# Performance work log

Hardware: AMD Instinct MI355X
Metric: run time of the kernel (lower is better)

## Reference

```python
import jax, jax.numpy as jnp
import numpy as np

N = 50000          # nodes
E = 800000         # edges (before self-loops)
F_IN, F_HID, F_OUT = 128, 64, 64
NEG_SLOPE_ATT = 0.2   # GATConv internal leaky_relu
NEG_SLOPE_ACT = 0.01  # F.leaky_relu default between layers


def setup_inputs() -> dict:
    key = jax.random.key(0)
    ks = jax.random.split(key, 16)

    def glorot(k, shape):
        fan = float(sum(shape)) if len(shape) > 1 else float(shape[0])
        return jax.random.normal(k, shape, jnp.float32) * (2.0 / fan) ** 0.5

    return {
        "x": jax.random.normal(ks[0], (N, F_IN), jnp.float32),
        "edge_index": jax.random.randint(ks[1], (2, E), 0, N, dtype=jnp.int64),
        "W1": glorot(ks[2], (F_IN, F_HID)),
        "a_src1": glorot(ks[3], (F_HID,)),
        "a_dst1": glorot(ks[4], (F_HID,)),
        "b1": jnp.zeros((F_HID,), jnp.float32),
        "W2": glorot(ks[5], (F_HID, F_HID)),
        "a_src2": glorot(ks[6], (F_HID,)),
        "a_dst2": glorot(ks[7], (F_HID,)),
        "b2": jnp.zeros((F_HID,), jnp.float32),
        "W3": glorot(ks[8], (F_HID, F_OUT)),
        "a_src3": glorot(ks[9], (F_OUT,)),
        "a_dst3": glorot(ks[10], (F_OUT,)),
        "b3": jnp.zeros((F_OUT,), jnp.float32),
    }


def gat_conv(h, src, dst, W, a_src, a_dst, b):
    # Single-head PyG GATConv: project, per-edge scores, segment softmax over dst, scatter-add.
    z = h @ W                              # [N, C]
    e_src = z @ a_src                      # [N]
    e_dst = z @ a_dst                      # [N]
    e = jax.nn.leaky_relu(e_src[src] + e_dst[dst], NEG_SLOPE_ATT)  # [E']
    m = jax.ops.segment_max(e, dst, num_segments=N)
    ex = jnp.exp(e - m[dst])
    denom = jax.ops.segment_sum(ex, dst, num_segments=N)
    alpha = ex / (denom[dst] + 1e-16)      # segment softmax (PyG adds 1e-16)
    out = jax.ops.segment_sum(alpha[:, None] * z[src], dst, num_segments=N) + b
    return out, alpha


def reference(x, edge_index, W1, a_src1, a_dst1, b1, W2, a_src2, a_dst2, b2, W3, a_src3, a_dst3, b3):
    # add_self_loops=True (GATConv default): append (i, i) for every node
    loops = jnp.arange(N, dtype=edge_index.dtype)
    ei = jnp.concatenate([edge_index, jnp.stack([loops, loops])], axis=1)  # [2, E+N]
    src, dst = ei[0], ei[1]

    h = x
    alpha = None
    for (W, asr, ads, b) in ((W1, a_src1, a_dst1, b1),
                             (W2, a_src2, a_dst2, b2),
                             (W3, a_src3, a_dst3, b3)):
        h, alpha = gat_conv(h, src, dst, W, asr, ads, b)
        h = jax.nn.leaky_relu(h, NEG_SLOPE_ACT)
    return (h, ei, alpha)
```

## Files before the change

### kernel.cpp

```cpp
#include <hip/hip_runtime.h>
#include <hip/hip_bf16.h>
#include <hip/hip_fp8.h>

#define NN 50000
#define EE 800000
#define E2 850000
#define F_IN 128
#define F_HID 64
#define NCHUNK ((NN + 255) / 256)
#define NTILE  ((NN + 63) / 64)
#define AGGB 2048

#define PNB 32
#define BCAP 32768
#define PCAP 128
#define PCHUNK 2048
#define PBLOCKS ((EE + PCHUNK - 1) / PCHUNK)
#define SLICEB 64

__device__ __forceinline__ unsigned char f32_to_fp8(float x) {
    __hip_fp8_e4m3 t(x);
    return t.__x;
}
__device__ __forceinline__ float fp8_to_f32(unsigned char b) {
    __hip_fp8_e4m3 t; t.__x = b;
    return (float)t;
}

#if defined(__has_builtin)
#  if __has_builtin(__builtin_amdgcn_cvt_f32_fp8)
#    define CVT_FP8(v, s) __builtin_amdgcn_cvt_f32_fp8((v), (s))
#  endif
#endif
#ifndef CVT_FP8
#  define CVT_FP8(v, s) fp8_to_f32(((v) >> (8 * (s))) & 255)
#endif

__global__ __launch_bounds__(256) void hist_part_kernel(const int* __restrict__ ei,
                                                        int* __restrict__ deg,
                                                        int* __restrict__ bin_cur,
                                                        unsigned long long* __restrict__ bins,
                                                        float* __restrict__ ei_out) {
    __shared__ unsigned long long buf[PNB * PCAP];
    __shared__ int cnt[PNB];
    __shared__ int basep[PNB];
    int tid = threadIdx.x;
    if (tid < PNB) cnt[tid] = 0;
    __syncthreads();

    int e0 = blockIdx.x * PCHUNK;
    int eend = e0 + PCHUNK; if (eend > EE) eend = EE;
    for (int e = e0 + tid; e < eend; e += 256) {
        int s = ei[e], d = ei[EE + e];
        atomicAdd(&deg[d], 1);
        ei_out[e]      = (float)s;
        ei_out[E2 + e] = (float)d;
        int b = (int)(((long long)d * PNB) / NN);
        unsigned long long pk = ((unsigned long long)(unsigned)d << 32) | (unsigned)s;
        int r = atomicAdd(&cnt[b], 1);
        if (r < PCAP) buf[b * PCAP + r] = pk;
        else {
            int p = atomicAdd(&bin_cur[b], 1);
            if (p < BCAP) bins[(size_t)b * BCAP + p] = pk;
        }
    }
    __syncthreads();
    if (tid < PNB) {
        int c = cnt[tid]; if (c > PCAP) c = PCAP;
        basep[tid] = c ? atomicAdd(&bin_cur[tid], c) : 0;
        cnt[tid] = c;
    }
    __syncthreads();
    for (int b = 0; b < PNB; ++b) {
        int c = cnt[b];
        int bb = basep[b];
        for (int i = tid; i < c; i += 256) {
            int p = bb + i;
            if (p < BCAP) bins[(size_t)b * BCAP + p] = buf[b * PCAP + i];
        }
    }
}

__global__ __launch_bounds__(256) void scan_part12(const int* __restrict__ deg,
                                                   int* __restrict__ csum,
                                                   int* __restrict__ ticket) {
    int i = blockIdx.x * 256 + threadIdx.x;
    int v = (i < NN) ? deg[i] + 1 : 0;
#pragma unroll
    for (int d = 32; d; d >>= 1) v += __shfl_xor(v, d);
    __shared__ int ws[4];
    if ((threadIdx.x & 63) == 0) ws[threadIdx.x >> 6] = v;
    __syncthreads();
    __shared__ int isLast;
    if (threadIdx.x == 0) {
        atomicExch(&csum[blockIdx.x], ws[0] + ws[1] + ws[2] + ws[3]);
        __threadfence();
        isLast = (atomicAdd(ticket, 1) == gridDim.x - 1) ? 1 : 0;
    }
    __syncthreads();
    if (isLast) {
        __threadfence();
        __shared__ int sd[256];
        int t = threadIdx.x;
        int v2 = (t < NCHUNK) ? atomicAdd(&csum[t], 0) : 0;
        sd[t] = v2;
        __syncthreads();
        for (int off = 1; off < 256; off <<= 1) {
            int o = (t >= off) ? sd[t - off] : 0;
            __syncthreads();
            sd[t] += o;
            __syncthreads();
        }
        if (t < NCHUNK) atomicExch(&csum[t], sd[t] - v2);
    }
}

__global__ __launch_bounds__(256) void scan_part3(const int* __restrict__ deg,
                                                  const int* __restrict__ csum,
                                                  int* __restrict__ offs,
                                                  int* __restrict__ cursor,
                                                  int* __restrict__ src_sorted,
                                                  float* __restrict__ ei_out) {
    __shared__ int sd[256];
    int t = threadIdx.x;
    int i = blockIdx.x * 256 + t;
    int v = (i < NN) ? deg[i] + 1 : 0;
    sd[t] = v;
    __syncthreads();
    for (int off = 1; off < 256; off <<= 1) {
        int o = (t >= off) ? sd[t - off] : 0;
        __syncthreads();
        sd[t] += o;
        __syncthreads();
    }
    if (i < NN) {
        int ex = sd[t] - v + csum[blockIdx.x];
        offs[i] = ex;
        cursor[i] = ex + 1;
        src_sorted[ex] = i;
        ei_out[EE + i]      = (float)i;
        ei_out[E2 + EE + i] = (float)i;
    }
}

__global__ __launch_bounds__(256) void scatter_bins(const int* __restrict__ bin_cur,
                                                    const unsigned long long* __restrict__ bins,
                                                    int* __restrict__ cursor,
                                                    int* __restrict__ src_sorted) {
    int b = blockIdx.x & (PNB - 1);
    int slice = blockIdx.x >> 5;
    int cnt = bin_cur[b];
    if (cnt > BCAP) cnt = BCAP;
    const unsigned long long* bp = bins + (size_t)b * BCAP;
    for (int i = slice * 256 + threadIdx.x; i < cnt; i += SLICEB * 256) {
        unsigned long long v = bp[i];
        int d = (int)(v >> 32);
        int s = (int)(v & 0xffffffffu);
        int pos = atomicAdd(&cursor[d], 1);
        src_sorted[pos] = s;
    }
}

template <int K>
__global__ __launch_bounds__(256) void gemm_tile(const float* __restrict__ h,
                                                 const float* __restrict__ W,
                                                 const float* __restrict__ a_src,
                                                 const float* __restrict__ a_dst,
                                                 unsigned char* __restrict__ z8,
                                                 float* __restrict__ es,
                                                 float* __restrict__ ed) {
    constexpr int LDA = K + 4;
    __shared__ float Alds[64 * LDA];
    __shared__ float Blds[K * 64];

    int tid = threadIdx.x;
    int base = blockIdx.x * 64;

    {
        constexpr int F4R = K / 4;
        for (int t = tid; t < 64 * F4R; t += 256) {
            int r = t / F4R;
            int c4 = t % F4R;
            int gr = base + r;
            if (gr >= NN) gr = NN - 1;
            float4 v = *(const float4*)(h + (size_t)gr * K + c4 * 4);
            *(float4*)(&Alds[r * LDA + c4 * 4]) = v;
        }
    }
    for (int t = tid; t < K * 16; t += 256) {
        float4 v = *(const float4*)(W + t * 4);
        *(float4*)(&Blds[t * 4]) = v;
    }
    __syncthreads();

    int tx = tid & 15;
    int ty = tid >> 4;

    float acc[4][4] = {};
#pragma unroll 4
    for (int k = 0; k < K; k += 4) {
        float4 a[4], b[4];
#pragma unroll
        for (int i = 0; i < 4; ++i)
            a[i] = *(const float4*)(&Alds[(4 * ty + i) * LDA + k]);
#pragma unroll
        for (int kk = 0; kk < 4; ++kk)
            b[kk] = *(const float4*)(&Blds[(k + kk) * 64 + 4 * tx]);
#pragma unroll
        for (int i = 0; i < 4; ++i) {
            acc[i][0] = fmaf(a[i].x, b[0].x, acc[i][0]);
            acc[i][1] = fmaf(a[i].x, b[0].y, acc[i][1]);
            acc[i][2] = fmaf(a[i].x, b[0].z, acc[i][2]);
            acc[i][3] = fmaf(a[i].x, b[0].w, acc[i][3]);
            acc[i][0] = fmaf(a[i].y, b[1].x, acc[i][0]);
            acc[i][1] = fmaf(a[i].y, b[1].y, acc[i][1]);
            acc[i][2] = fmaf(a[i].y, b[1].z, acc[i][2]);
            acc[i][3] = fmaf(a[i].y, b[1].w, acc[i][3]);
            acc[i][0] = fmaf(a[i].z, b[2].x, acc[i][0]);
            acc[i][1] = fmaf(a[i].z, b[2].y, acc[i][1]);
            acc[i][2] = fmaf(a[i].z, b[2].z, acc[i][2]);
            acc[i][3] = fmaf(a[i].z, b[2].w, acc[i][3]);
            acc[i][0] = fmaf(a[i].w, b[3].x, acc[i][0]);
            acc[i][1] = fmaf(a[i].w, b[3].y, acc[i][1]);
            acc[i][2] = fmaf(a[i].w, b[3].z, acc[i][2]);
            acc[i][3] = fmaf(a[i].w, b[3].w, acc[i][3]);
        }
    }

    float4 as4 = *(const float4*)(a_src + 4 * tx);
    float4 ad4 = *(const float4*)(a_dst + 4 * tx);
    float ps[4], pd[4];
#pragma unroll
    for (int i = 0; i < 4; ++i) {
        int gr = base + 4 * ty + i;
        if (gr < NN) {
            unsigned int pk = (unsigned int)f32_to_fp8(acc[i][0])
                            | ((unsigned int)f32_to_fp8(acc[i][1]) << 8)
                            | ((unsigned int)f32_to_fp8(acc[i][2]) << 16)
                            | ((unsigned int)f32_to_fp8(acc[i][3]) << 24);
            *(unsigned int*)(&z8[(size_t)gr * 64 + 4 * tx]) = pk;
        }
        ps[i] = acc[i][0] * as4.x + acc[i][1] * as4.y + acc[i][2] * as4.z + acc[i][3] * as4.w;
        pd[i] = acc[i][0] * ad4.x + acc[i][1] * ad4.y + acc[i][2] * ad4.z + acc[i][3] * ad4.w;
    }
#pragma unroll
    for (int d = 1; d < 16; d <<= 1) {
#pragma unroll
        for (int i = 0; i < 4; ++i) {
            ps[i] += __shfl_xor(ps[i], d);
            pd[i] += __shfl_xor(pd[i], d);
        }
    }
    if (tx == 0) {
#pragma unroll
        for (int i = 0; i < 4; ++i) {
            int gr = base + 4 * ty + i;
            if (gr < NN) { es[gr] = ps[i]; ed[gr] = pd[i]; }
        }
    }
}

__global__ __launch_bounds__(256) void aggregate(const int* __restrict__ offs,
                                                 const int* __restrict__ deg,
                                                 const int* __restrict__ src_sorted,
                                                 const float* __restrict__ es,
                                                 const float* __restrict__ ed,
                                                 const unsigned char* __restrict__ z8,
                                                 const float* __restrict__ bias,
                                                 float* __restrict__ hout,
                                                 float* __restrict__ denom_out) {
    int tid = threadIdx.x;
    int lane = tid & 63;
    int wave = blockIdx.x * 4 + (tid >> 6);
    const int NW = AGGB * 4;

    int sub  = lane >> 4;
    int fgrp = (lane & 15) * 4;
    const unsigned char* zp = z8 + fgrp;
    float4 bi4 = *(const float4*)(bias + fgrp);

    int n = wave;
    if (n >= NN) return;
    n = __builtin_amdgcn_readfirstlane(n);
    int off = offs[n];
    int dg = deg[n] + 1;
    float edn = ed[n];
    int sv = src_sorted[off + ((lane < dg) ? lane : 0)];
    float ese = es[sv];

    while (true) {
        int n2 = n + NW;
        bool more = (n2 < NN);
        int off2 = 0, dg2 = 0; float edn2 = 0.f;
        if (more) {
            n2 = __builtin_amdgcn_readfirstlane(n2);
            off2 = offs[n2]; dg2 = deg[n2] + 1; edn2 = ed[n2];
        }

        float dsum = 0.f;
        float a0 = 0.f, a1 = 0.f, a2 = 0.f, a3 = 0.f;
        for (int b0 = 0; b0 < dg; b0 += 64) {
            int bl = dg - b0; if (bl > 64) bl = 64;
            int svb; float esv;
            if (b0 == 0) { svb = sv; esv = ese; }
            else {
                svb = src_sorted[off + b0 + ((lane < bl) ? lane : 0)];
                esv = es[svb];
            }
            float e = esv + edn;
            e = (e > 0.f) ? e : 0.2f * e;
            float w = (lane < bl) ? __expf(e) : 0.f;
            dsum += w;

            int ng = (bl + 3) >> 2;
            int j = 0;
            for (; j + 4 <= ng; j += 4) {
                int i0 = 4 * j + sub;
                int   s0 = __shfl(svb, i0);
                int   s1 = __shfl(svb, i0 + 4);
                int   s2 = __shfl(svb, i0 + 8);
                int   s3 = __shfl(svb, i0 + 12);
                unsigned int v0 = *(const unsigned int*)(zp + (size_t)s0 * 64);
                unsigned int v1 = *(const unsigned int*)(zp + (size_t)s1 * 64);
                unsigned int v2 = *(const unsigned int*)(zp + (size_t)s2 * 64);
                unsigned int v3 = *(const unsigned int*)(zp + (size_t)s3 * 64);
                float w0 = __shfl(w, i0);
                float w1 = __shfl(w, i0 + 4);
                float w2 = __shfl(w, i0 + 8);
                float w3 = __shfl(w, i0 + 12);
                a0 = fmaf(w0, CVT_FP8(v0, 0), a0);
                a1 = fmaf(w0, CVT_FP8(v0, 1), a1);
                a2 = fmaf(w0, CVT_FP8(v0, 2), a2);
                a3 = fmaf(w0, CVT_FP8(v0, 3), a3);
                a0 = fmaf(w1, CVT_FP8(v1, 0), a0);
                a1 = fmaf(w1, CVT_FP8(v1, 1), a1);
                a2 = fmaf(w1, CVT_FP8(v1, 2), a2);
                a3 = fmaf(w1, CVT_FP8(v1, 3), a3);
                a0 = fmaf(w2, CVT_FP8(v2, 0), a0);
                a1 = fmaf(w2, CVT_FP8(v2, 1), a1);
                a2 = fmaf(w2, CVT_FP8(v2, 2), a2);
                a3 = fmaf(w2, CVT_FP8(v2, 3), a3);
                a0 = fmaf(w3, CVT_FP8(v3, 0), a0);
                a1 = fmaf(w3, CVT_FP8(v3, 1), a1);
                a2 = fmaf(w3, CVT_FP8(v3, 2), a2);
                a3 = fmaf(w3, CVT_FP8(v3, 3), a3);
            }
            for (; j < ng; ++j) {
                int i0 = 4 * j + sub;
                int   s0 = __shfl(svb, i0);
                unsigned int v0 = *(const unsigned int*)(zp + (size_t)s0 * 64);
                float w0 = __shfl(w, i0);
                a0 = fmaf(w0, CVT_FP8(v0, 0), a0);
                a1 = fmaf(w0, CVT_FP8(v0, 1), a1);
                a2 = fmaf(w0, CVT_FP8(v0, 2), a2);
                a3 = fmaf(w0, CVT_FP8(v0, 3), a3);
            }
        }

        int sv2 = 0;
        if (more) sv2 = src_sorted[off2 + ((lane < dg2) ? lane : 0)];

        a0 += __shfl_xor(a0, 16); a1 += __shfl_xor(a1, 16);
        a2 += __shfl_xor(a2, 16); a3 += __shfl_xor(a3, 16);
        a0 += __shfl_xor(a0, 32); a1 += __shfl_xor(a1, 32);
        a2 += __shfl_xor(a2, 32); a3 += __shfl_xor(a3, 32);
#pragma unroll
        for (int d = 32; d; d >>= 1) dsum += __shfl_xor(dsum, d);

        float ese2 = 0.f;
        if (more) ese2 = es[sv2];

        float inv = 1.f / (dsum + 1e-16f);
        if (lane < 16) {
            float4 o;
            o.x = a0 * inv + bi4.x;
            o.y = a1 * inv + bi4.y;
            o.z = a2 * inv + bi4.z;
            o.w = a3 * inv + bi4.w;
            o.x = (o.x > 0.f) ? o.x : 0.01f * o.x;
            o.y = (o.y > 0.f) ? o.y : 0.01f * o.y;
            o.z = (o.z > 0.f) ? o.z : 0.01f * o.z;
            o.w = (o.w > 0.f) ? o.w : 0.01f * o.w;
            *(float4*)(hout + (size_t)n * 64 + fgrp) = o;
        }
        if (lane == 0) denom_out[n] = dsum;

        if (!more) break;
        n = n2; off = off2; dg = dg2; edn = edn2; sv = sv2; ese = ese2;
    }
}

__global__ __launch_bounds__(256) void alpha_kernel(const int* __restrict__ ei,
                                                    const float* __restrict__ es,
                                                    const float* __restrict__ ed,
                                                    const float* __restrict__ denom,
                                                    float* __restrict__ alpha_out) {
    int e = blockIdx.x * 256 + threadIdx.x;
    if (e >= E2) return;
    int s, d;
    if (e < EE) { s = ei[e]; d = ei[EE + e]; }
    else        { s = d = e - EE; }
    float x = es[s] + ed[d];
    x = (x > 0.f) ? x : 0.2f * x;
    alpha_out[e] = __expf(x) / (denom[d] + 1e-16f);
}

extern "C" void kernel_launch(void* const* d_in, const int* in_sizes, int n_in,
                              void* d_out, int out_size, void* d_ws, size_t ws_size,
                              hipStream_t stream) {
    const float* x   = (const float*)d_in[0];
    const int*   ei  = (const int*)d_in[1];
    const float* W1  = (const float*)d_in[2];
    const float* as1 = (const float*)d_in[3];
    const float* ad1 = (const float*)d_in[4];
    const float* b1  = (const float*)d_in[5];
    const float* W2  = (const float*)d_in[6];
    const float* as2 = (const float*)d_in[7];
    const float* ad2 = (const float*)d_in[8];
    const float* b2  = (const float*)d_in[9];
    const float* W3  = (const float*)d_in[10];
    const float* as3 = (const float*)d_in[11];
    const float* ad3 = (const float*)d_in[12];
    const float* b3  = (const float*)d_in[13];

    float* out       = (float*)d_out;
    float* h_out     = out;
    float* ei_out    = out + (size_t)NN * 64;
    float* alpha_out = ei_out + 2 * (size_t)E2;

    char* w = (char*)d_ws;
    auto carve = [&](size_t bytes) {
        void* p = (void*)w;
        w += (bytes + 255) & ~size_t(255);
        return p;
    };
    float* h1  = (float*)carve((size_t)NN * 64 * 4);
    float* h2  = (float*)carve((size_t)NN * 64 * 4);
    unsigned char* z8 = (unsigned char*)carve((size_t)NN * 64);
    float* es  = (float*)carve((size_t)NN * 4);
    float* ed  = (float*)carve((size_t)NN * 4);
    float* denom = (float*)carve((size_t)NN * 4);
    int* deg        = (int*)carve(((size_t)NN + 64) * 4);
    int* ticket     = deg + NN;
    int* bin_cur    = deg + NN + 1;
    int* offs       = (int*)carve((size_t)NN * 4);
    int* cursor     = (int*)carve((size_t)NN * 4);
    int* csum       = (int*)carve((size_t)NCHUNK * 4);
    int* src_sorted = (int*)carve((size_t)E2 * 4);
    unsigned long long* bins = (unsigned long long*)carve((size_t)PNB * BCAP * 8);

    const int EB = (E2 + 255) / 256;

    hipMemsetAsync(deg, 0, ((size_t)NN + 64) * 4, stream);
    hist_part_kernel<<<PBLOCKS, 256, 0, stream>>>(ei, deg, bin_cur, bins, ei_out);
    scan_part12<<<NCHUNK, 256, 0, stream>>>(deg, csum, ticket);
    scan_part3<<<NCHUNK, 256, 0, stream>>>(deg, csum, offs, cursor, src_sorted, ei_out);
    scatter_bins<<<PNB * SLICEB, 256, 0, stream>>>(bin_cur, bins, cursor, src_sorted);

    gemm_tile<F_IN><<<NTILE, 256, 0, stream>>>(x, W1, as1, ad1, z8, es, ed);
    aggregate<<<AGGB, 256, 0, stream>>>(offs, deg, src_sorted, es, ed, z8, b1, h1, denom);
    gemm_tile<F_HID><<<NTILE, 256, 0, stream>>>(h1, W2, as2, ad2, z8, es, ed);
    aggregate<<<AGGB, 256, 0, stream>>>(offs, deg, src_sorted, es, ed, z8, b2, h2, denom);
    gemm_tile<F_HID><<<NTILE, 256, 0, stream>>>(h2, W3, as3, ad3, z8, es, ed);
    aggregate<<<AGGB, 256, 0, stream>>>(offs, deg, src_sorted, es, ed, z8, b3, h_out, denom);
    alpha_kernel<<<EB, 256, 0, stream>>>(ei, es, ed, denom, alpha_out);
}
```

Measured before the change: 305.6 us.

## Split degree counting into bin-local pass and shrink partition chunks

The edge partition kernel no longer does global atomics on degree. A new count_bins kernel reads the already-binned edges per destination range and does the degree atomics there, so the atomics land in a localized address range. The partition kernel uses smaller chunks (512 edges, 48-slot LDS buffers) to get more blocks and less LDS per block. The flush loop is flattened with a prefix sum and binary search so all threads stay busy. The cost is one extra kernel launch and a second read of the bins array.

Measured after the change: 315.6 us. +3.2%, slower.

```diff
diff --git a/kernel.cpp b/kernel.cpp
--- a/kernel.cpp
+++ b/kernel.cpp
@@ -13,9 +13,9 @@
 
 #define PNB 32
 #define BCAP 32768
-#define PCAP 128
-#define PCHUNK 2048
-#define PBLOCKS ((EE + PCHUNK - 1) / PCHUNK)
+#define CBCH 512
+#define CBB ((EE + CBCH - 1) / CBCH)
+#define CBCAP 48
 #define SLICEB 64
 
 __device__ __forceinline__ unsigned char f32_to_fp8(float x) {
@@ -36,29 +36,28 @@
 #  define CVT_FP8(v, s) fp8_to_f32(((v) >> (8 * (s))) & 255)
 #endif
 
-__global__ __launch_bounds__(256) void hist_part_kernel(const int* __restrict__ ei,
-                                                        int* __restrict__ deg,
-                                                        int* __restrict__ bin_cur,
-                                                        unsigned long long* __restrict__ bins,
-                                                        float* __restrict__ ei_out) {
-    __shared__ unsigned long long buf[PNB * PCAP];
+__global__ __launch_bounds__(256) void cast_bin_kernel(const int* __restrict__ ei,
+                                                       int* __restrict__ bin_cur,
+                                                       unsigned long long* __restrict__ bins,
+                                                       float* __restrict__ ei_out) {
+    __shared__ unsigned long long buf[PNB * CBCAP];
     __shared__ int cnt[PNB];
-    __shared__ int basep[PNB];
+    __shared__ int gbase[PNB];
+    __shared__ int pfx[PNB + 1];
     int tid = threadIdx.x;
     if (tid < PNB) cnt[tid] = 0;
     __syncthreads();
 
-    int e0 = blockIdx.x * PCHUNK;
-    int eend = e0 + PCHUNK; if (eend > EE) eend = EE;
-    for (int e = e0 + tid; e < eend; e += 256) {
+    int e0 = blockIdx.x * CBCH;
+    int e1 = e0 + CBCH; if (e1 > EE) e1 = EE;
+    for (int e = e0 + tid; e < e1; e += 256) {
         int s = ei[e], d = ei[EE + e];
-        atomicAdd(&deg[d], 1);
         ei_out[e]      = (float)s;
         ei_out[E2 + e] = (float)d;
         int b = (int)(((long long)d * PNB) / NN);
         unsigned long long pk = ((unsigned long long)(unsigned)d << 32) | (unsigned)s;
         int r = atomicAdd(&cnt[b], 1);
-        if (r < PCAP) buf[b * PCAP + r] = pk;
+        if (r < CBCAP) buf[b * CBCAP + r] = pk;
         else {
             int p = atomicAdd(&bin_cur[b], 1);
             if (p < BCAP) bins[(size_t)b * BCAP + p] = pk;
@@ -66,18 +65,38 @@
     }
     __syncthreads();
     if (tid < PNB) {
-        int c = cnt[tid]; if (c > PCAP) c = PCAP;
-        basep[tid] = c ? atomicAdd(&bin_cur[tid], c) : 0;
+        int c = cnt[tid]; if (c > CBCAP) c = CBCAP;
         cnt[tid] = c;
-    }
-    __syncthreads();
-    for (int b = 0; b < PNB; ++b) {
-        int c = cnt[b];
-        int bb = basep[b];
-        for (int i = tid; i < c; i += 256) {
-            int p = bb + i;
-            if (p < BCAP) bins[(size_t)b * BCAP + p] = buf[b * PCAP + i];
-        }
+        gbase[tid] = c ? atomicAdd(&bin_cur[tid], c) : 0;
+    }
+    __syncthreads();
+    if (tid == 0) {
+        int run = 0;
+        for (int b = 0; b < PNB; ++b) { pfx[b] = run; run += cnt[b]; }
+        pfx[PNB] = run;
+    }
+    __syncthreads();
+    int total = pfx[PNB];
+    for (int idx = tid; idx < total; idx += 256) {
+        int lo = 0, hi = PNB;
+        while (hi - lo > 1) { int mid = (lo + hi) >> 1; if (pfx[mid] <= idx) lo = mid; else hi = mid; }
+        int b = lo, li = idx - pfx[b];
+        int p = gbase[b] + li;
+        if (p < BCAP) bins[(size_t)b * BCAP + p] = buf[b * CBCAP + li];
+    }
+}
+
+__global__ __launch_bounds__(256) void count_bins(const int* __restrict__ bin_cur,
+                                                  const unsigned long long* __restrict__ bins,
+                                                  int* __restrict__ deg) {
+    int b = blockIdx.x & (PNB - 1);
+    int slice = blockIdx.x >> 5;
+    int cnt = bin_cur[b];
+    if (cnt > BCAP) cnt = BCAP;
+    const unsigned long long* bp = bins + (size_t)b * BCAP;
+    for (int i = slice * 256 + threadIdx.x; i < cnt; i += SLICEB * 256) {
+        int d = (int)(bp[i] >> 32);
+        atomicAdd(&deg[d], 1);
     }
 }
 
@@ -452,7 +471,8 @@
     const int EB = (E2 + 255) / 256;
 
     hipMemsetAsync(deg, 0, ((size_t)NN + 64) * 4, stream);
-    hist_part_kernel<<<PBLOCKS, 256, 0, stream>>>(ei, deg, bin_cur, bins, ei_out);
+    cast_bin_kernel<<<CBB, 256, 0, stream>>>(ei, bin_cur, bins, ei_out);
+    count_bins<<<PNB * SLICEB, 256, 0, stream>>>(bin_cur, bins, deg);
     scan_part12<<<NCHUNK, 256, 0, stream>>>(deg, csum, ticket);
     scan_part3<<<NCHUNK, 256, 0, stream>>>(deg, csum, offs, cursor, src_sorted, ei_out);
     scatter_bins<<<PNB * SLICEB, 256, 0, stream>>>(bin_cur, bins, cursor, src_sorted);
```
